# Optimization experiments

Hardware: AMD Instinct MI355X
Metric: run time of the kernel (lower is better)

The kernel has to match this reference:

```python
import jax, jax.numpy as jnp
import numpy as np

NUM_HEADS = 16
DIM = 1024
HID = DIM // NUM_HEADS
B, S = 2, 2048
NEG_INF = -1e30


def setup_inputs() -> dict:
    key = jax.random.key(0)
    ks = jax.random.split(key, 8)
    def xavier(k, shape, fan_in, fan_out):
        limit = np.sqrt(6.0 / (fan_in + fan_out))
        return jax.random.uniform(k, shape, jnp.float32, -limit, limit)
    return {
        "q": jax.random.normal(ks[0], (B, S, DIM), jnp.float32),
        "k": jax.random.normal(ks[1], (B, S, DIM), jnp.float32),
        "v": jax.random.normal(ks[2], (B, S, DIM), jnp.float32),
        "Wq": xavier(ks[3], (1, NUM_HEADS, DIM, HID), DIM, HID),
        "Wk": xavier(ks[4], (1, NUM_HEADS, DIM, HID), DIM, HID),
        "Wv": xavier(ks[5], (1, NUM_HEADS, DIM, HID), DIM, HID),
        "Wo": xavier(ks[6], (1, DIM, DIM), DIM, DIM),
        "mask": jax.random.randint(ks[7], (B, S), 0, 2, jnp.int32),
    }


def reference(q, k, v, Wq, Wk, Wv, Wo, mask):
    b, s, d = q.shape
    norm = jnp.sqrt(jnp.asarray(HID, q.dtype))
    # per-head projections: [B,S,D] x [H,D,hd] -> [B,H,S,hd]
    qh = jnp.einsum('bsd,hde->bhse', q, Wq[0])
    kh = jnp.einsum('bsd,hde->bhse', k, Wk[0])
    vh = jnp.einsum('bsd,hde->bhse', v, Wv[0])
    scores = jnp.einsum('bhse,bhte->bhst', qh, kh) / norm  # [B,H,S,S]
    m = mask.astype(bool)
    # original fills masked rows AND cols with 0.0 (not -inf)
    pad = m[:, None, :, None] | m[:, None, None, :]
    scores = jnp.where(pad, 0.0, scores)
    causal = jnp.triu(jnp.ones((s, s), bool), 1)
    scores = jnp.where(causal, NEG_INF, scores)
    attn = jax.nn.softmax(scores, axis=-1)
    out = jnp.einsum('bhst,bhte->bhse', attn, vh)  # [B,H,S,hd]
    # faithful to original: raw view (memory reinterpretation), NO head transpose
    out = out.reshape(b, s, NUM_HEADS * HID)
    return out @ Wo[0]
```

## Files before the change

### kernel.cpp

```cpp
#include <hip/hip_runtime.h>
#include <hip/hip_bf16.h>

#define BB 2
#define SS 2048
#define DD 1024
#define HH 16
#define HD 64

typedef __attribute__((ext_vector_type(8))) short bf16x8;
typedef __attribute__((ext_vector_type(4))) float floatx4;

__device__ __forceinline__ short f2bf(float x) {
  __hip_bfloat16 h = __float2bfloat16(x);
  return __builtin_bit_cast(short, h);
}

__device__ __forceinline__ unsigned cvtpk_bf16(float lo, float hi) {
  unsigned r;
  asm("v_cvt_pk_bf16_f32 %0, %1, %2" : "=v"(r) : "v"(lo), "v"(hi));
  return r;
}

__device__ __forceinline__ void load_lds16(const void* g, void* l) {
  __builtin_amdgcn_global_load_lds(
      (const __attribute__((address_space(1))) unsigned int*)g,
      (__attribute__((address_space(3))) unsigned int*)l, 16, 0, 0);
}

__device__ __forceinline__ float redsum16(float v) {
  v += __shfl_xor(v, 1, 64);
  v += __shfl_xor(v, 2, 64);
  v += __shfl_xor(v, 4, 64);
  v += __shfl_xor(v, 8, 64);
  return v;
}

__global__ __launch_bounds__(256) void prep(
    const float* __restrict__ q, const float* __restrict__ k,
    const float* __restrict__ v, const float* __restrict__ Wq,
    const float* __restrict__ Wk, const float* __restrict__ Wv,
    const float* __restrict__ Wo, short* __restrict__ qo,
    short* __restrict__ ko, short* __restrict__ vo, short* __restrict__ qT,
    short* __restrict__ kT, short* __restrict__ vT, short* __restrict__ WoT) {
  __shared__ short sT[64 * 72];
  const int blk = blockIdx.x;
  if (blk < 12288) {
    const int which = blk >> 12, x = blk & 4095;
    const float* src = which == 0 ? q : which == 1 ? k : v;
    short* dst       = which == 0 ? qo : which == 1 ? ko : vo;
    size_t i = ((size_t)x * 256 + threadIdx.x) * 4;
    float4 f = *(const float4*)(src + i);
    short4 s;
    s.x = f2bf(f.x); s.y = f2bf(f.y); s.z = f2bf(f.z); s.w = f2bf(f.w);
    *(short4*)(dst + i) = s;
    return;
  }
  const int t = threadIdx.x, r = t >> 2, c0 = (t & 3) * 16;
  const float* src;
  short* dst;
  if (blk < 13056) {
    const int b2 = blk - 12288, which = b2 >> 8, rr = b2 & 255;
    const int dtile = rr & 15, h = rr >> 4, d0 = dtile * 64;
    const float* W = which == 0 ? Wq : which == 1 ? Wk : Wv;
    short* WT      = which == 0 ? qT : which == 1 ? kT : vT;
    src = W + ((size_t)h * DD + d0 + r) * HD + c0;
    dst = WT + ((size_t)h * HD + r) * DD + d0 + c0;
  } else {
    const int b3 = blk - 13056;
    const int k0 = (b3 & 15) * 64, n0 = (b3 >> 4) * 64;
    src = Wo + (size_t)(k0 + r) * DD + n0 + c0;
    dst = WoT + (size_t)(n0 + r) * DD + k0 + c0;
  }
  const float4* s4 = (const float4*)src;
  float4 f0 = s4[0], f1 = s4[1], f2 = s4[2], f3 = s4[3];
  const float ff[16] = {f0.x, f0.y, f0.z, f0.w, f1.x, f1.y, f1.z, f1.w,
                        f2.x, f2.y, f2.z, f2.w, f3.x, f3.y, f3.z, f3.w};
#pragma unroll
  for (int j = 0; j < 16; ++j) sT[r * 72 + c0 + j] = f2bf(ff[j]);
  __syncthreads();
  alignas(16) short tmp[16];
#pragma unroll
  for (int j = 0; j < 16; ++j) tmp[j] = sT[(c0 + j) * 72 + r];
  *(int4*)(dst) = *(const int4*)(tmp);
  *(int4*)(dst + 8) = *(const int4*)(tmp + 8);
}

__global__ __launch_bounds__(256) void proj(
    const short* __restrict__ xq, const short* __restrict__ xk,
    const short* __restrict__ xv, const short* __restrict__ WqT,
    const short* __restrict__ WkT, const short* __restrict__ WvT,
    const int* __restrict__ mask, short* __restrict__ qh,
    short* __restrict__ kh, short* __restrict__ vhT) {
  __shared__ short sA[128 * 32];
  __shared__ short sB[128 * 32];
  __shared__ short sT2[128 * 136];
  const int xcd = blockIdx.x & 7, tt = blockIdx.x >> 3;
  const int which = tt >> 5;
  const int rest = tt & 31;
  const int j = ((xcd & 3) << 1) | (rest >> 4);
  const int i = ((xcd >> 2) << 4) | (rest & 15);
  const short* X  = which == 0 ? xq : which == 1 ? xk : xv;
  const short* WT = which == 0 ? WqT : which == 1 ? WkT : WvT;
  const int m0 = i * 128, n0 = j * 128;
  const int tid = threadIdx.x, wid = tid >> 6, lane = tid & 63;
  const int quad = lane >> 4, l16 = lane & 15;
  const int wr = wid >> 1, wc = wid & 1;

  floatx4 acc[4][4] = {};
  for (int k0 = 0; k0 < DD; k0 += 32) {
    __syncthreads();
#pragma unroll
    for (int ii = 0; ii < 2; ++ii) {
      const int c = wid * 2 + ii;
      const int ci = c * 64 + lane;
      load_lds16(X + (size_t)(m0 + (ci >> 2)) * DD + k0 + (ci & 3) * 8,
                 &sA[c * 512]);
      load_lds16(WT + (size_t)(n0 + (ci >> 2)) * DD + k0 + (ci & 3) * 8,
                 &sB[c * 512]);
    }
    __syncthreads();
    bf16x8 af[4], bfr[4];
#pragma unroll
    for (int mi = 0; mi < 4; ++mi)
      af[mi] = *(const bf16x8*)&sA[(wr * 64 + mi * 16 + l16) * 32 + quad * 8];
#pragma unroll
    for (int ni = 0; ni < 4; ++ni)
      bfr[ni] = *(const bf16x8*)&sB[(wc * 64 + ni * 16 + l16) * 32 + quad * 8];
#pragma unroll
    for (int mi = 0; mi < 4; ++mi)
#pragma unroll
      for (int ni = 0; ni < 4; ++ni)
        acc[mi][ni] = __builtin_amdgcn_mfma_f32_16x16x32_bf16(
            af[mi], bfr[ni], acc[mi][ni], 0, 0, 0);
  }
  if (which != 2) {
    short* dst = which == 0 ? qh : kh;
    const float scale = (which == 0) ? 0.18033688f : 1.0f;
#pragma unroll
    for (int mi = 0; mi < 4; ++mi)
#pragma unroll
      for (int r2 = 0; r2 < 4; ++r2) {
        const int m = m0 + wr * 64 + mi * 16 + quad * 4 + r2;
        const float rs = mask[m] ? 0.f : scale;
#pragma unroll
        for (int ni = 0; ni < 4; ++ni) {
          const int n = n0 + wc * 64 + ni * 16 + l16;
          dst[(size_t)m * DD + n] = f2bf(acc[mi][ni][r2] * rs);
        }
      }
  } else {
    __syncthreads();
#pragma unroll
    for (int mi = 0; mi < 4; ++mi)
#pragma unroll
      for (int ni = 0; ni < 4; ++ni)
#pragma unroll
        for (int r2 = 0; r2 < 4; ++r2) {
          const int ml = wr * 64 + mi * 16 + quad * 4 + r2;
          const int nl = wc * 64 + ni * 16 + l16;
          sT2[nl * 136 + ml] = f2bf(acc[mi][ni][r2]);
        }
    __syncthreads();
    const int b = m0 >> 11;
    const int row = tid >> 1, half = tid & 1;
    const int h = (n0 + row) >> 6, e = (n0 + row) & 63;
    short* dstp = vhT + ((size_t)(b * HH + h) * HD + e) * SS + (m0 & 2047) +
                  half * 64;
    const short* srcl = &sT2[row * 136 + half * 64];
#pragma unroll
    for (int jj = 0; jj < 8; ++jj)
      *(int4*)(dstp + jj * 8) = *(const int4*)(srcl + jj * 8);
  }
}

__global__ __launch_bounds__(256, 2) void attn(
    const short* __restrict__ qh, const short* __restrict__ kh,
    const short* __restrict__ vhT, short* __restrict__ X) {
  __shared__ short sm[16384 + 4 * 1152];
  const int tid = threadIdx.x, wid = tid >> 6, lane = tid & 63;
  const int quad = lane >> 4, l16 = lane & 15;
  const int xcd = blockIdx.x & 7, slot = blockIdx.x >> 3;
  const int bh = (xcd << 2) | (slot & 3);
  const int iblk = 31 - (slot >> 2);
  const int nt = iblk + 1;
  const int b = bh >> 4, h = bh & 15;
  const int r0 = iblk * 64;
  const int wrow = r0 + wid * 16;

  const short* Q  = qh + (size_t)b * SS * DD + h * HD;
  const short* K  = kh + (size_t)b * SS * DD + h * HD;
  const short* Vt = vhT + (size_t)bh * HD * SS;
  short* sPw = &sm[16384 + wid * 1152];
  const int swz = (l16 & 7) << 3;

  const int sr0 = tid >> 3, ss0 = (tid & 7) ^ (sr0 & 7);
  const int sr1 = (tid + 256) >> 3, ss1 = (tid & 7) ^ (sr1 & 7);
  const short* pK0 = K + (size_t)sr0 * DD + ss0 * 8;
  const short* pK1 = K + (size_t)sr1 * DD + ss1 * 8;
  const short* pV0 = Vt + (size_t)sr0 * SS + ss0 * 8;
  const short* pV1 = Vt + (size_t)sr1 * SS + ss1 * 8;

  auto stage = [&](int buf, int t) {
    const size_t ko = (size_t)t * 64 * DD;
    const int tc = t * 64;
    short* base = &sm[buf * 8192];
    load_lds16(pK0 + ko, base + tid * 8);
    load_lds16(pK1 + ko, base + 2048 + tid * 8);
    load_lds16(pV0 + tc, base + 4096 + tid * 8);
    load_lds16(pV1 + tc, base + 6144 + tid * 8);
  };

  bf16x8 aq[2];
#pragma unroll
  for (int ks = 0; ks < 2; ++ks)
    aq[ks] = *(const bf16x8*)(Q + (size_t)(wrow + l16) * DD + ks * 32 +
                              quad * 8);

  floatx4 o[4] = {};
  float lacc[4] = {};

  stage(0, 0);
  __syncthreads();
  int cur = 0;
  for (int t = 0; t < nt; ++t) {
    if (t + 1 < nt) stage(cur ^ 1, t + 1);
    const short* kb = &sm[cur * 8192];
    const short* vb = kb + 4096;
    bf16x8 bk[4][2];
#pragma unroll
    for (int ni = 0; ni < 4; ++ni)
#pragma unroll
      for (int ks = 0; ks < 2; ++ks)
        bk[ni][ks] = *(const bf16x8*)&kb[(ni * 16 + l16) * 64 +
                                         ((ks * 32 + quad * 8) ^ swz)];
    floatx4 s[4] = {};
#pragma unroll
    for (int ks = 0; ks < 2; ++ks)
#pragma unroll
      for (int ni = 0; ni < 4; ++ni)
        s[ni] = __builtin_amdgcn_mfma_f32_16x16x32_bf16(aq[ks], bk[ni][ks],
                                                        s[ni], 0, 0, 0);
    const bool diag = (t == nt - 1);
    const int t0 = t * 64;
#pragma unroll
    for (int ni = 0; ni < 4; ++ni)
#pragma unroll
      for (int r2p = 0; r2p < 2; ++r2p) {
        float p0 = __builtin_amdgcn_exp2f(s[ni][2 * r2p]);
        float p1 = __builtin_amdgcn_exp2f(s[ni][2 * r2p + 1]);
        if (diag) {
          const int row = wrow + quad * 4 + 2 * r2p;
          const int col = t0 + ni * 16 + l16;
          if (col > row) p0 = 0.f;
          if (col > row + 1) p1 = 0.f;
        }
        lacc[2 * r2p] += p0;
        lacc[2 * r2p + 1] += p1;
        const unsigned pk = cvtpk_bf16(p0, p1);
        short* wp = &sPw[(quad * 4 + 2 * r2p) * 72 + ni * 16 + l16];
        wp[0] = (short)pk;
        wp[72] = (short)(pk >> 16);
      }
#pragma unroll
    for (int ks = 0; ks < 2; ++ks) {
      const bf16x8 ap =
          *(const bf16x8*)&sPw[l16 * 72 + ks * 32 + quad * 8];
#pragma unroll
      for (int ei = 0; ei < 4; ++ei) {
        const bf16x8 bv = *(const bf16x8*)&vb[(ei * 16 + l16) * 64 +
                                              ((ks * 32 + quad * 8) ^ swz)];
        o[ei] = __builtin_amdgcn_mfma_f32_16x16x32_bf16(ap, bv, o[ei], 0, 0,
                                                        0);
      }
    }
    __syncthreads();
    cur ^= 1;
  }

#pragma unroll
  for (int r2 = 0; r2 < 4; ++r2) {
    const float inv = 1.0f / redsum16(lacc[r2]);
    const int srow = wrow + quad * 4 + r2;
#pragma unroll
    for (int ei = 0; ei < 4; ++ei)
      X[((size_t)bh * SS + srow) * HD + ei * 16 + l16] =
          f2bf(o[ei][r2] * inv);
  }
}

__global__ __launch_bounds__(256) void oproj(const short* __restrict__ X,
                                             const short* __restrict__ WoT,
                                             float* __restrict__ out) {
  __shared__ short sA[128 * 32];
  __shared__ short sB[64 * 32];
  const int m0 = blockIdx.x * 128, n0 = blockIdx.y * 64;
  const int tid = threadIdx.x, wid = tid >> 6, lane = tid & 63;
  const int quad = lane >> 4, l16 = lane & 15;
  const int wr = wid >> 1, wc = wid & 1;

  floatx4 acc[4][2] = {};
  for (int k0 = 0; k0 < DD; k0 += 32) {
    __syncthreads();
#pragma unroll
    for (int i = 0; i < 2; ++i) {
      const int c = wid * 2 + i;
      const int ci = c * 64 + lane;
      load_lds16(X + (size_t)(m0 + (ci >> 2)) * DD + k0 + (ci & 3) * 8,
                 &sA[c * 512]);
    }
    {
      const int ci = wid * 64 + lane;
      load_lds16(WoT + (size_t)(n0 + (ci >> 2)) * DD + k0 + (ci & 3) * 8,
                 &sB[wid * 512]);
    }
    __syncthreads();
    bf16x8 af[4], bfr[2];
#pragma unroll
    for (int mi = 0; mi < 4; ++mi)
      af[mi] = *(const bf16x8*)&sA[(wr * 64 + mi * 16 + l16) * 32 + quad * 8];
#pragma unroll
    for (int ni = 0; ni < 2; ++ni)
      bfr[ni] = *(const bf16x8*)&sB[(wc * 32 + ni * 16 + l16) * 32 + quad * 8];
#pragma unroll
    for (int mi = 0; mi < 4; ++mi)
#pragma unroll
      for (int ni = 0; ni < 2; ++ni)
        acc[mi][ni] = __builtin_amdgcn_mfma_f32_16x16x32_bf16(
            af[mi], bfr[ni], acc[mi][ni], 0, 0, 0);
  }
#pragma unroll
  for (int mi = 0; mi < 4; ++mi)
#pragma unroll
    for (int ni = 0; ni < 2; ++ni)
#pragma unroll
      for (int r2 = 0; r2 < 4; ++r2)
        out[(size_t)(m0 + wr * 64 + mi * 16 + quad * 4 + r2) * DD + n0 +
            wc * 32 + ni * 16 + l16] = acc[mi][ni][r2];
}

extern "C" void kernel_launch(void* const* d_in, const int* in_sizes, int n_in,
                              void* d_out, int out_size, void* d_ws,
                              size_t ws_size, hipStream_t stream) {
  const float* q  = (const float*)d_in[0];
  const float* k  = (const float*)d_in[1];
  const float* v  = (const float*)d_in[2];
  const float* Wq = (const float*)d_in[3];
  const float* Wk = (const float*)d_in[4];
  const float* Wv = (const float*)d_in[5];
  const float* Wo = (const float*)d_in[6];
  const int* mask = (const int*)d_in[7];
  float* out = (float*)d_out;

  short* ws = (short*)d_ws;
  const size_t NIN = (size_t)BB * SS * DD;
  const size_t NWH = (size_t)HH * HD * DD;
  short* qb  = ws;
  short* kb  = ws + NIN;
  short* vb  = ws + 2 * NIN;
  short* WqT = ws + 3 * NIN;
  short* WkT = WqT + NWH;
  short* WvT = WkT + NWH;
  short* WoT = WvT + NWH;
  short* qhp = WoT + (size_t)DD * DD;
  short* khp = qhp + NIN;
  short* vhT = khp + NIN;
  short* Xp  = qb;

  prep<<<dim3(13312), 256, 0, stream>>>(q, k, v, Wq, Wk, Wv, Wo, qb, kb, vb,
                                        WqT, WkT, WvT, WoT);
  proj<<<dim3(768), 256, 0, stream>>>(qb, kb, vb, WqT, WkT, WvT, mask, qhp,
                                      khp, vhT);
  attn<<<dim3(1024), 256, 0, stream>>>(qhp, khp, vhT, Xp);
  oproj<<<dim3(32, 16), 256, 0, stream>>>(Xp, WoT, out);
}
```

Baseline: 215.8 us.

## Double-buffer LDS staging in projection GEMMs and shrink V transpose buffer

Both the QKV projection and output projection GEMMs now use two LDS buffers. The global-to-LDS load for the next K slice is issued before computing on the current one, and only one barrier per iteration remains. The V-transpose scratch is aliased with the staging buffers in a union and the transpose is done in two 64-column passes, so total LDS stays small enough to preserve occupancy. The cost is the extra LDS for the second buffer and a more serialized two-pass transpose epilogue.

```diff
diff --git a/kernel.cpp b/kernel.cpp
--- a/kernel.cpp
+++ b/kernel.cpp
@@ -91,9 +91,13 @@
     const short* __restrict__ WkT, const short* __restrict__ WvT,
     const int* __restrict__ mask, short* __restrict__ qh,
     short* __restrict__ kh, short* __restrict__ vhT) {
-  __shared__ short sA[128 * 32];
-  __shared__ short sB[128 * 32];
-  __shared__ short sT2[128 * 136];
+  __shared__ union {
+    struct {
+      short A[2][128 * 32];
+      short B[2][128 * 32];
+    } s;
+    short tr[64 * 136];
+  } u;
   const int xcd = blockIdx.x & 7, tt = blockIdx.x >> 3;
   const int which = tt >> 5;
   const int rest = tt & 31;
@@ -106,33 +110,45 @@
   const int quad = lane >> 4, l16 = lane & 15;
   const int wr = wid >> 1, wc = wid & 1;
 
-  floatx4 acc[4][4] = {};
-  for (int k0 = 0; k0 < DD; k0 += 32) {
-    __syncthreads();
+  auto stage = [&](int buf, int k0) {
 #pragma unroll
     for (int ii = 0; ii < 2; ++ii) {
       const int c = wid * 2 + ii;
       const int ci = c * 64 + lane;
       load_lds16(X + (size_t)(m0 + (ci >> 2)) * DD + k0 + (ci & 3) * 8,
-                 &sA[c * 512]);
+                 &u.s.A[buf][c * 512]);
       load_lds16(WT + (size_t)(n0 + (ci >> 2)) * DD + k0 + (ci & 3) * 8,
-                 &sB[c * 512]);
+                 &u.s.B[buf][c * 512]);
     }
-    __syncthreads();
+  };
+
+  floatx4 acc[4][4] = {};
+  stage(0, 0);
+  __syncthreads();
+  int cur = 0;
+  for (int k0 = 0; k0 < DD; k0 += 32) {
+    if (k0 + 32 < DD) stage(cur ^ 1, k0 + 32);
     bf16x8 af[4], bfr[4];
 #pragma unroll
     for (int mi = 0; mi < 4; ++mi)
-      af[mi] = *(const bf16x8*)&sA[(wr * 64 + mi * 16 + l16) * 32 + quad * 8];
+      af[mi] =
+          *(const bf16x8*)&u.s.A[cur][(wr * 64 + mi * 16 + l16) * 32 +
+                                      quad * 8];
 #pragma unroll
     for (int ni = 0; ni < 4; ++ni)
-      bfr[ni] = *(const bf16x8*)&sB[(wc * 64 + ni * 16 + l16) * 32 + quad * 8];
+      bfr[ni] =
+          *(const bf16x8*)&u.s.B[cur][(wc * 64 + ni * 16 + l16) * 32 +
+                                      quad * 8];
 #pragma unroll
     for (int mi = 0; mi < 4; ++mi)
 #pragma unroll
       for (int ni = 0; ni < 4; ++ni)
         acc[mi][ni] = __builtin_amdgcn_mfma_f32_16x16x32_bf16(
             af[mi], bfr[ni], acc[mi][ni], 0, 0, 0);
-  }
+    __syncthreads();
+    cur ^= 1;
+  }
+
   if (which != 2) {
     short* dst = which == 0 ? qh : kh;
     const float scale = (which == 0) ? 0.18033688f : 1.0f;
@@ -149,27 +165,33 @@
         }
       }
   } else {
-    __syncthreads();
-#pragma unroll
-    for (int mi = 0; mi < 4; ++mi)
-#pragma unroll
-      for (int ni = 0; ni < 4; ++ni)
-#pragma unroll
-        for (int r2 = 0; r2 < 4; ++r2) {
-          const int ml = wr * 64 + mi * 16 + quad * 4 + r2;
-          const int nl = wc * 64 + ni * 16 + l16;
-          sT2[nl * 136 + ml] = f2bf(acc[mi][ni][r2]);
-        }
-    __syncthreads();
     const int b = m0 >> 11;
-    const int row = tid >> 1, half = tid & 1;
-    const int h = (n0 + row) >> 6, e = (n0 + row) & 63;
-    short* dstp = vhT + ((size_t)(b * HH + h) * HD + e) * SS + (m0 & 2047) +
-                  half * 64;
-    const short* srcl = &sT2[row * 136 + half * 64];
-#pragma unroll
-    for (int jj = 0; jj < 8; ++jj)
-      *(int4*)(dstp + jj * 8) = *(const int4*)(srcl + jj * 8);
+#pragma unroll
+    for (int p = 0; p < 2; ++p) {
+      if (wc == p) {
+#pragma unroll
+        for (int mi = 0; mi < 4; ++mi)
+#pragma unroll
+          for (int ni = 0; ni < 4; ++ni)
+#pragma unroll
+            for (int r2 = 0; r2 < 4; ++r2) {
+              const int ml = wr * 64 + mi * 16 + quad * 4 + r2;
+              const int nl = ni * 16 + l16;
+              u.tr[nl * 136 + ml] = f2bf(acc[mi][ni][r2]);
+            }
+      }
+      __syncthreads();
+      const int row = tid >> 2, part = tid & 3;
+      const int gn = n0 + p * 64 + row;
+      const int h = gn >> 6, e = gn & 63;
+      short* dstp = vhT + ((size_t)(b * HH + h) * HD + e) * SS + (m0 & 2047) +
+                    part * 32;
+      const short* srcl = &u.tr[row * 136 + part * 32];
+#pragma unroll
+      for (int jj = 0; jj < 4; ++jj)
+        *(int4*)(dstp + jj * 8) = *(const int4*)(srcl + jj * 8);
+      if (p == 0) __syncthreads();
+    }
   }
 }
 
@@ -291,42 +313,51 @@
 __global__ __launch_bounds__(256) void oproj(const short* __restrict__ X,
                                              const short* __restrict__ WoT,
                                              float* __restrict__ out) {
-  __shared__ short sA[128 * 32];
-  __shared__ short sB[64 * 32];
+  __shared__ short sA[2][128 * 32];
+  __shared__ short sB[2][64 * 32];
   const int m0 = blockIdx.x * 128, n0 = blockIdx.y * 64;
   const int tid = threadIdx.x, wid = tid >> 6, lane = tid & 63;
   const int quad = lane >> 4, l16 = lane & 15;
   const int wr = wid >> 1, wc = wid & 1;
 
-  floatx4 acc[4][2] = {};
-  for (int k0 = 0; k0 < DD; k0 += 32) {
-    __syncthreads();
+  auto stage = [&](int buf, int k0) {
 #pragma unroll
     for (int i = 0; i < 2; ++i) {
       const int c = wid * 2 + i;
       const int ci = c * 64 + lane;
       load_lds16(X + (size_t)(m0 + (ci >> 2)) * DD + k0 + (ci & 3) * 8,
-                 &sA[c * 512]);
+                 &sA[buf][c * 512]);
     }
     {
       const int ci = wid * 64 + lane;
       load_lds16(WoT + (size_t)(n0 + (ci >> 2)) * DD + k0 + (ci & 3) * 8,
-                 &sB[wid * 512]);
+                 &sB[buf][wid * 512]);
     }
-    __syncthreads();
+  };
+
+  floatx4 acc[4][2] = {};
+  stage(0, 0);
+  __syncthreads();
+  int cur = 0;
+  for (int k0 = 0; k0 < DD; k0 += 32) {
+    if (k0 + 32 < DD) stage(cur ^ 1, k0 + 32);
     bf16x8 af[4], bfr[2];
 #pragma unroll
     for (int mi = 0; mi < 4; ++mi)
-      af[mi] = *(const bf16x8*)&sA[(wr * 64 + mi * 16 + l16) * 32 + quad * 8];
+      af[mi] = *(const bf16x8*)&sA[cur][(wr * 64 + mi * 16 + l16) * 32 +
+                                        quad * 8];
 #pragma unroll
     for (int ni = 0; ni < 2; ++ni)
-      bfr[ni] = *(const bf16x8*)&sB[(wc * 32 + ni * 16 + l16) * 32 + quad * 8];
+      bfr[ni] = *(const bf16x8*)&sB[cur][(wc * 32 + ni * 16 + l16) * 32 +
+                                         quad * 8];
 #pragma unroll
     for (int mi = 0; mi < 4; ++mi)
 #pragma unroll
       for (int ni = 0; ni < 2; ++ni)
         acc[mi][ni] = __builtin_amdgcn_mfma_f32_16x16x32_bf16(
             af[mi], bfr[ni], acc[mi][ni], 0, 0, 0);
+    __syncthreads();
+    cur ^= 1;
   }
 #pragma unroll
   for (int mi = 0; mi < 4; ++mi)
```

Result: no change. 211.8 us (-1.9%).
